# Performance work log

Measured on AMD Instinct MI355X. Metric: run time of the kernel, lower is better.

The kernel has to match this reference:

```python
import jax, jax.numpy as jnp
import numpy as np

B, F, FO, J, H, IN, OUT = 256, 16, 32, 22, 8, 256, 512
HID = OUT // H    # 64
HS = HID // 2     # 32 (spatial/temporal half)
NEG = -1e9


def setup_inputs() -> dict:
    key = jax.random.key(0)
    ks = jax.random.split(key, 10)
    s = 0.02
    f32 = jnp.float32
    return {
        "q": jax.random.normal(ks[0], (B, FO, J, IN), f32),
        "k": jax.random.normal(ks[1], (B, F, J, IN), f32),
        "v": jax.random.normal(ks[2], (B, F, J, IN), f32),
        "mask_s": jax.random.randint(ks[3], (J, J), 0, 2, jnp.int32),
        "mask_t": jax.random.randint(ks[4], (FO, FO), 0, 2, jnp.int32),
        "Wq_w": jax.random.normal(ks[5], (IN, OUT), f32) * s,
        "Wq_b": jnp.zeros((OUT,), f32),
        "Wk_w": jax.random.normal(ks[6], (IN, OUT), f32) * s,
        "Wk_b": jnp.zeros((OUT,), f32),
        "Wv_w": jax.random.normal(ks[7], (IN, OUT), f32) * s,
        "Wv_b": jnp.zeros((OUT,), f32),
        "conv_s_w": jax.random.normal(ks[8], (FO, F), f32) * s,  # 1x1 Conv2d over frame channels
        "conv_s_b": jnp.zeros((FO,), f32),
        "conv_t_w": jax.random.normal(ks[9], (FO, F), f32) * s,
        "conv_t_b": jnp.zeros((FO,), f32),
    }


def _forward(q, k, v, mask_s, mask_t, Wq_w, Wq_b, Wk_w, Wk_b, Wv_w, Wv_b,
             conv_s_w, conv_s_b, conv_t_w, conv_t_b):
    b = q.shape[0]
    temporal_size = q.shape[1]  # torch: q.shape[1] AFTER Wq -> num_frames_out
    q = q @ Wq_w + Wq_b
    k = k @ Wk_w + Wk_b
    v = v @ Wv_w + Wv_b
    # raw reshapes, exactly as the torch module (not a standard head split)
    q = q.reshape(b, H, FO, J, HID)
    k = k.reshape(b, H, F, J, HID)
    v = v.reshape(b, H, F, J, HID)
    q_s, q_t = q[..., :HS], q[..., HS:]
    k_s, k_t = k[..., :HS], k[..., HS:]
    v_s, v_t = v[..., :HS], v[..., HS:]

    def explode_s(x):
        # (b,H,F,J,HS) -> merge heads into channels -> 1x1 conv over frames -> (b,H,FO,J,HS)
        x = x.transpose(0, 2, 3, 1, 4).reshape(b, F, J, H * HS)
        x = jnp.einsum('of,bfjc->bojc', conv_s_w, x) + conv_s_b[None, :, None, None]
        return x.reshape(b, FO, J, H, HS).transpose(0, 3, 1, 2, 4)

    k_s = explode_s(k_s)
    v_s = explode_s(v_s)

    q_t = q_t.transpose(0, 1, 3, 2, 4)  # (b,H,J,FO,HS)
    v_t = v_t.transpose(0, 1, 3, 2, 4)  # (b,H,J,F,HS)
    kt = k_t.reshape(b * H, F, J, HS)   # torch double-permute is identity
    kt = jnp.einsum('of,nfjc->nojc', conv_t_w, kt) + conv_t_b[None, :, None, None]
    k_t = kt.reshape(b, H, FO, J, HS).transpose(0, 1, 3, 2, 4)  # (b,H,J,FO,HS)

    # faithful to torch.einsum: no shared contraction index -> outer product of sums
    attn_s = jnp.einsum('bhtsc,bhtdu->bhtsu', q_s, jnp.swapaxes(k_s, 3, 4))  # (b,H,FO,J,J)
    attn_s = jnp.where(mask_s == 0, NEG, attn_s)
    attn_t = jnp.einsum('bhstf,bhsug->bhstg', q_t, jnp.swapaxes(k_t, 3, 4))  # (b,H,J,FO,FO)
    attn_t = jnp.where(mask_t == 0, NEG, attn_t)
    attn_s = jax.nn.softmax(attn_s, axis=-1)
    attn_t = jax.nn.softmax(attn_t, axis=-1)

    # 'bhtss' takes the diagonal over the two joint axes (torch semantics)
    x_s = jnp.einsum('bhtss,bhtuf->bhtsf', attn_s, v_s)          # (b,H,FO,J,HS)
    x_t = jnp.einsum('bhstf,bhsug->bhstg', attn_t, v_t)          # (b,H,J,FO,HS)
    x_t = x_t.transpose(0, 1, 3, 2, 4)                            # (b,H,FO,J,HS)

    x_up = jnp.concatenate([x_s[:, :, :temporal_size], x_t], axis=-1)
    x_after_s = x_s[:, :, temporal_size:]                         # empty when q covers FO frames
    x_after = jnp.concatenate([x_after_s, jnp.zeros_like(x_after_s)], axis=-1)
    x = jnp.concatenate([x_up, x_after], axis=2)
    x = x.transpose(0, 2, 3, 1, 4).reshape(b, FO, J, H * HID)
    return x


def reference(q, k, v, mask_s, mask_t, Wq_w, Wq_b, Wk_w, Wk_b, Wv_w, Wv_b,
              conv_s_w, conv_s_b, conv_t_w, conv_t_b):
    return _forward(q, k, v, mask_s, mask_t, Wq_w, Wq_b, Wk_w, Wk_b, Wv_w, Wv_b,
                    conv_s_w, conv_s_b, conv_t_w, conv_t_b)
```

## Files before the change

kernel.cpp:

```cpp
#include <hip/hip_runtime.h>


#define NEGV (-1000000000.0f)

typedef __attribute__((ext_vector_type(8))) short short8;
typedef __attribute__((ext_vector_type(4))) float f32x4;

__device__ inline ushort f2bf(float f) {
  union { float f; unsigned u; } a;
  a.f = f;
  unsigned u = a.u;
  return (ushort)((u + 0x7FFFu + ((u >> 16) & 1u)) >> 16);
}

#define PUTG(g, pa, pb)                                                        \
  {                                                                            \
    int row_ = (g) >> 5, gl_ = (g) & 31;                                       \
    int gp_ = gl_ ^ (row_ & 7);                                                \
    short8 u_;                                                                 \
    u_[0] = (short)f2bf(pa[0]); u_[1] = (short)f2bf(pa[1]);                    \
    u_[2] = (short)f2bf(pa[2]); u_[3] = (short)f2bf(pa[3]);                    \
    u_[4] = (short)f2bf(pb[0]); u_[5] = (short)f2bf(pb[1]);                    \
    u_[6] = (short)f2bf(pb[2]); u_[7] = (short)f2bf(pb[3]);                    \
    *reinterpret_cast<short8*>(&lA[row_ * 256 + gp_ * 8]) = u_;                \
  }

#define STAGE44_NT(SRCPTR)                                                     \
  {                                                                            \
    const float* vsrc_ = (SRCPTR);                                             \
    int g0 = tid, g1 = tid + 512, g2 = tid + 1024;                             \
    f32x4 a0 = __builtin_nontemporal_load(                                     \
        reinterpret_cast<const f32x4*>(vsrc_ + g0 * 8));                       \
    f32x4 b0 = __builtin_nontemporal_load(                                     \
        reinterpret_cast<const f32x4*>(vsrc_ + g0 * 8 + 4));                   \
    f32x4 a1 = __builtin_nontemporal_load(                                     \
        reinterpret_cast<const f32x4*>(vsrc_ + g1 * 8));                       \
    f32x4 b1 = __builtin_nontemporal_load(                                     \
        reinterpret_cast<const f32x4*>(vsrc_ + g1 * 8 + 4));                   \
    f32x4 a2 = {0, 0, 0, 0}, b2 = {0, 0, 0, 0};                                \
    if (g2 < 1408) {                                                           \
      a2 = __builtin_nontemporal_load(                                         \
          reinterpret_cast<const f32x4*>(vsrc_ + g2 * 8));                     \
      b2 = __builtin_nontemporal_load(                                         \
          reinterpret_cast<const f32x4*>(vsrc_ + g2 * 8 + 4));                 \
    }                                                                          \
    PUTG(g0, a0, b0);                                                          \
    PUTG(g1, a1, b1);                                                          \
    if (g2 < 1408) PUTG(g2, a2, b2);                                           \
    if (tid < 128) {                                                           \
      int g = 1408 + tid;                                                      \
      int row_ = g >> 5, gp_ = (g & 31) ^ (row_ & 7);                          \
      short8 z = {0, 0, 0, 0, 0, 0, 0, 0};                                     \
      *reinterpret_cast<short8*>(&lA[row_ * 256 + gp_ * 8]) = z;               \
    }                                                                          \
  }

__global__ __launch_bounds__(512) void prep_all_kernel(const float* __restrict__ Wq_w,
                                                       const float* __restrict__ Wq_b,
                                                       const float* __restrict__ Wk_w,
                                                       const float* __restrict__ Wk_b,
                                                       const float* __restrict__ Wv_w,
                                                       ushort* __restrict__ qwf,
                                                       ushort* __restrict__ kwf,
                                                       ushort* __restrict__ wvtf,
                                                       float* __restrict__ sqb,
                                                       float* __restrict__ skb) {
  int bx = blockIdx.x, tid = threadIdx.x;
  if (bx < 256) {
    int idx = bx * 512 + tid;
    int e = idx & 7;
    int lane = (idx >> 3) & 63;
    int ks = (idx >> 9) & 7;
    int nt = idx >> 12;
    int r0 = lane & 15, kb = lane >> 4;
    int k = ks * 32 + kb * 8 + e;
    int ch = nt * 16 + r0;
    wvtf[idx] = f2bf(Wv_w[k * 512 + ch]);
  } else if (bx < 272) {
    int idx = (bx - 256) * 512 + tid;
    int which = idx >> 12;
    int r = idx & 4095;
    int e = r & 7;
    int lane = (r >> 3) & 63;
    int ks = r >> 9;
    int m = lane & 15, kb = lane >> 4;
    int k = ks * 32 + kb * 8 + e;
    float s = 0.f;
    if (m < 8) {
      const float* W = which ? Wk_w : Wq_w;
      const float4* p = reinterpret_cast<const float4*>(W + (size_t)k * 512 + m * 64);
      #pragma unroll
      for (int c4 = 0; c4 < 8; ++c4) {
        float4 x = p[c4];
        s += x.x + x.y + x.z + x.w;
      }
    }
    (which ? kwf : qwf)[r] = f2bf(s);
  } else {
    if (tid < 8) {
      float s = 0.f;
      for (int c = 0; c < 32; ++c) s += Wq_b[tid * 64 + c];
      sqb[tid] = s;
    } else if (tid < 16) {
      int mm = tid - 8;
      float s = 0.f;
      for (int c = 0; c < 32; ++c) s += Wk_b[mm * 64 + c];
      skb[mm] = s;
    }
  }
}

__global__ __launch_bounds__(512, 2) void fused2_kernel(const float* __restrict__ q,
                                                        const float* __restrict__ k,
                                                        const float* __restrict__ v,
                                                        const ushort* __restrict__ qwf,
                                                        const ushort* __restrict__ kwf,
                                                        const ushort* __restrict__ wvtf,
                                                        const float* __restrict__ sqb,
                                                        const float* __restrict__ skb,
                                                        const float* __restrict__ Wv_b,
                                                        float* __restrict__ qsum,
                                                        float* __restrict__ ksumraw,
                                                        float* __restrict__ vs_inner,
                                                        float* __restrict__ vtsum) {
  int bx = blockIdx.x;
  __shared__ float sbuf[6656];
  int tid = threadIdx.x, lane = tid & 63, w = tid >> 6;
  int r0 = lane & 15, kb = lane >> 4;

  bool isQK = (bx >= 4096) || !(bx & 1);
  if (isQK) {
    int gid = (bx >= 4096) ? (2048 + bx - 4096) : (bx >> 1);
    int tile = gid * 8 + w;
    bool isK = tile >= 11264;
    int tt = isK ? tile - 11264 : tile;
    const float* src = (isK ? k : q) + (size_t)(tt * 16 + r0) * 256;
    const ushort* wf = isK ? kwf : qwf;
    f32x4 acc = {0.f, 0.f, 0.f, 0.f};
    #pragma unroll
    for (int ks = 0; ks < 8; ++ks) {
      f32x4 xa = __builtin_nontemporal_load(
          reinterpret_cast<const f32x4*>(src + ks * 32 + kb * 8));
      f32x4 xb = __builtin_nontemporal_load(
          reinterpret_cast<const f32x4*>(src + ks * 32 + kb * 8 + 4));
      short8 a;
      a[0] = (short)f2bf(xa[0]); a[1] = (short)f2bf(xa[1]);
      a[2] = (short)f2bf(xa[2]); a[3] = (short)f2bf(xa[3]);
      a[4] = (short)f2bf(xb[0]); a[5] = (short)f2bf(xb[1]);
      a[6] = (short)f2bf(xb[2]); a[7] = (short)f2bf(xb[3]);
      short8 bf = *reinterpret_cast<const short8*>(wf + (ks * 64 + lane) * 8);
      acc = __builtin_amdgcn_mfma_f32_16x16x32_bf16(a, bf, acc, 0, 0, 0);
    }
    if (r0 < 8) {
      int m = r0;
      float bias = isK ? skb[m] : sqb[m];
      #pragma unroll
      for (int reg = 0; reg < 4; ++reg) {
        int R = tt * 16 + kb * 4 + reg;
        if (!isK) {
          int b = R / 704, rem = R % 704;
          int fo2 = rem / 22, j2 = rem % 22;
          int lf = (fo2 & 3) * 11264 + j2 * 512 + m * 64;
          int t = lf / 1408;
          int s = (lf % 1408) >> 6;
          int h = fo2 >> 2;
          qsum[(((size_t)b * 8 + h) * 32 + t) * 22 + s] = acc[reg] + bias;
        } else {
          int b = R / 352, rem = R % 352;
          int f2 = rem / 22, j2 = rem % 22;
          int lf = (f2 & 1) * 11264 + j2 * 512 + m * 64;
          int floc = lf / 1408;
          int jj = (lf % 1408) >> 6;
          int h = f2 >> 1;
          ksumraw[(((size_t)b * 8 + h) * 16 + floc) * 22 + jj] = acc[reg] + bias;
        }
      }
    }
  } else {
    int bh = bx >> 1;
    ushort* lA = reinterpret_cast<ushort*>(sbuf);
    float* dump = sbuf;
    STAGE44_NT(v + (size_t)bh * 11264);
    __syncthreads();

    int nt0 = w * 4;
    f32x4 acc[3][4];
    #pragma unroll
    for (int m = 0; m < 3; ++m)
      #pragma unroll
      for (int n = 0; n < 4; ++n) acc[m][n] = (f32x4){0.f, 0.f, 0.f, 0.f};

    #pragma unroll
    for (int ks = 0; ks < 8; ++ks) {
      int go = ((ks * 4 + kb) ^ (r0 & 7)) * 8;
      short8 a0 = *reinterpret_cast<const short8*>(&lA[(r0) * 256 + go]);
      short8 a1 = *reinterpret_cast<const short8*>(&lA[(16 + r0) * 256 + go]);
      short8 a2 = *reinterpret_cast<const short8*>(&lA[(32 + r0) * 256 + go]);
      #pragma unroll
      for (int n = 0; n < 4; ++n) {
        short8 bf = *reinterpret_cast<const short8*>(
            wvtf + ((size_t)((nt0 + n) * 8 + ks) * 64 + lane) * 8);
        acc[0][n] = __builtin_amdgcn_mfma_f32_16x16x32_bf16(bf, a0, acc[0][n], 0, 0, 0);
        acc[1][n] = __builtin_amdgcn_mfma_f32_16x16x32_bf16(bf, a1, acc[1][n], 0, 0, 0);
        acc[2][n] = __builtin_amdgcn_mfma_f32_16x16x32_bf16(bf, a2, acc[2][n], 0, 0, 0);
      }
    }
    __syncthreads();

    #pragma unroll
    for (int n = 0; n < 4; ++n) {
      float4 bq = *reinterpret_cast<const float4*>(Wv_b + w * 64 + n * 16 + kb * 4);
      int dbase = tid * 13;
      #pragma unroll
      for (int m = 0; m < 3; ++m) {
        dump[dbase + m * 4 + 0] = acc[m][n][0] + bq.x;
        dump[dbase + m * 4 + 1] = acc[m][n][1] + bq.y;
        dump[dbase + m * 4 + 2] = acc[m][n][2] + bq.z;
        dump[dbase + m * 4 + 3] = acc[m][n][3] + bq.w;
      }
      __syncthreads();
      if (n < 2) {
        if (tid < 256) {
          int f = tid >> 4, rest = tid & 15;
          int kb2 = rest >> 2, reg = rest & 3;
          float s = 0.f;
          #pragma unroll
          for (int u = 0; u < 22; ++u) {
            int fj = f * 22 + u;
            int f2 = (fj >= 176) ? 1 : 0;
            int rem = fj - f2 * 176;
            int j = rem >> 3, ww = rem & 7;
            int vrow = f2 * 22 + j;
            int m = vrow >> 4, rr = vrow & 15;
            s += dump[(ww * 64 + kb2 * 16 + rr) * 13 + m * 4 + reg];
          }
          vs_inner[(size_t)bh * 512 + f * 32 + n * 16 + kb2 * 4 + reg] = s;
        }
      } else {
        if (tid < 352) {
          int jj = tid >> 4, rest = tid & 15;
          int kb2 = rest >> 2, reg = rest & 3;
          float s = 0.f;
          #pragma unroll
          for (int f = 0; f < 16; ++f) {
            int fj = f * 22 + jj;
            int f2 = (fj >= 176) ? 1 : 0;
            int rem = fj - f2 * 176;
            int j = rem >> 3, ww = rem & 7;
            int vrow = f2 * 22 + j;
            int m = vrow >> 4, rr = vrow & 15;
            s += dump[(ww * 64 + kb2 * 16 + rr) * 13 + m * 4 + reg];
          }
          vtsum[(size_t)bh * 704 + jj * 32 + (n - 2) * 16 + kb2 * 4 + reg] = s;
        }
      }
      __syncthreads();
    }
  }
}

__global__ __launch_bounds__(512, 2) void final2_kernel(const float* __restrict__ qsum,
                                                        const float* __restrict__ ksumraw,
                                                        const float* __restrict__ vs_inner,
                                                        const float* __restrict__ vtsum,
                                                        const int* __restrict__ mask_s,
                                                        const float* __restrict__ csw,
                                                        const float* __restrict__ csb,
                                                        float* __restrict__ out) {
  int blk = blockIdx.x;
  int b = blk & 255, tp = blk >> 8;
  int t0 = tp * 2;
  __shared__ float vtl[8][704];
  __shared__ float vsi[8][16][32];
  __shared__ float kraw[8][16][22];
  __shared__ float ql2[2][8][22];
  __shared__ float klrow[2][8][22];
  __shared__ float vss[2][8][32];
  __shared__ float dg2[2][8][22];
  __shared__ float lcw[2][18];
  __shared__ int msk[484];
  int tid = threadIdx.x;
  size_t bb = (size_t)b;

  {
    const float4* p = reinterpret_cast<const float4*>(vtsum + bb * 5632);
    float4* dst = reinterpret_cast<float4*>(&vtl[0][0]);
    for (int i = tid; i < 1408; i += 512) dst[i] = p[i];
  }
  {
    const float4* p = reinterpret_cast<const float4*>(vs_inner + bb * 4096);
    float4* dst = reinterpret_cast<float4*>(&vsi[0][0][0]);
    for (int i = tid; i < 1024; i += 512) dst[i] = p[i];
  }
  {
    const float4* p = reinterpret_cast<const float4*>(ksumraw + bb * 2816);
    float4* dst = reinterpret_cast<float4*>(&kraw[0][0][0]);
    for (int i = tid; i < 704; i += 512) dst[i] = p[i];
  }
  if (tid < 352) {
    int tt = tid / 176, r = tid % 176;
    int h = r / 22, s = r % 22;
    ql2[tt][h][s] = qsum[((bb * 8 + h) * 32 + t0 + tt) * 22 + s];
  }
  if (tid < 484) msk[tid] = mask_s[tid];
  if (tid < 32) {
    int tt = tid >> 4, f = tid & 15;
    lcw[tt][f] = csw[(t0 + tt) * 16 + f];
  }
  if (tid >= 32 && tid < 34) lcw[tid - 32][16] = csb[t0 + (tid - 32)];
  __syncthreads();

  if (tid < 352) {
    int tt = tid / 176, r = tid % 176;
    int h = r / 22, j = r % 22;
    float a = 32.0f * lcw[tt][16];
    #pragma unroll
    for (int f = 0; f < 16; ++f) a += lcw[tt][f] * kraw[h][f][j];
    klrow[tt][h][j] = a;
  }
  {
    int tt = tid >> 8, r = tid & 255;
    int h = r >> 5, d = r & 31;
    float a = 22.0f * lcw[tt][16];
    #pragma unroll
    for (int f = 0; f < 16; ++f) a += lcw[tt][f] * vsi[h][f][d];
    vss[tt][h][d] = a;
  }
  __syncthreads();

  if (tid < 352) {
    int tt = tid / 176, r = tid % 176;
    int h = r / 22, s = r % 22;
    float qv = ql2[tt][h][s];
    float mx = -3.0e38f;
    #pragma unroll
    for (int u = 0; u < 22; ++u) {
      float av = msk[s * 22 + u] ? qv * klrow[tt][h][u] : NEGV;
      mx = fmaxf(mx, av);
    }
    float den = 0.f;
    #pragma unroll
    for (int u = 0; u < 22; ++u) {
      float av = msk[s * 22 + u] ? qv * klrow[tt][h][u] : NEGV;
      den += expf(av - mx);
    }
    float as = msk[s * 22 + s] ? qv * klrow[tt][h][s] : NEGV;
    dg2[tt][h][s] = expf(as - mx) / den;
  }
  __syncthreads();

  #pragma unroll
  for (int tt = 0; tt < 2; ++tt) {
    f32x4* ob4 = reinterpret_cast<f32x4*>(out + (size_t)(b * 32 + t0 + tt) * 11264);
    #pragma unroll
    for (int it = 0; it < 6; ++it) {
      int i4 = tid + it * 512;
      if (i4 < 2816) {
        int s = i4 >> 7;
        int ch4 = i4 & 127;
        int h = ch4 >> 4;
        int d0 = (ch4 & 15) * 4;
        f32x4 val;
        if (d0 < 32) {
          float g = dg2[tt][h][s];
          const float* vp = &vss[tt][h][d0];
          val[0] = g * vp[0]; val[1] = g * vp[1]; val[2] = g * vp[2]; val[3] = g * vp[3];
        } else {
          const float* tpn = &vtl[h][s * 32 + d0 - 32];
          val[0] = tpn[0]; val[1] = tpn[1]; val[2] = tpn[2]; val[3] = tpn[3];
        }
        __builtin_nontemporal_store(val, &ob4[i4]);
      }
    }
  }
}

extern "C" void kernel_launch(void* const* d_in, const int* in_sizes, int n_in,
                              void* d_out, int out_size, void* d_ws, size_t ws_size,
                              hipStream_t stream) {
  const float* q = (const float*)d_in[0];
  const float* k = (const float*)d_in[1];
  const float* v = (const float*)d_in[2];
  const int* mask_s = (const int*)d_in[3];
  const float* Wq_w = (const float*)d_in[5];
  const float* Wq_b = (const float*)d_in[6];
  const float* Wk_w = (const float*)d_in[7];
  const float* Wk_b = (const float*)d_in[8];
  const float* Wv_w = (const float*)d_in[9];
  const float* Wv_b = (const float*)d_in[10];
  const float* csw = (const float*)d_in[11];
  const float* csb = (const float*)d_in[12];
  float* out = (float*)d_out;

  float* ws = (float*)d_ws;
  float* sqb = ws;
  float* skb = ws + 8;
  ushort* wvtf = (ushort*)(ws + 16);
  ushort* qwf = (ushort*)(ws + 65552);
  ushort* kwf = (ushort*)(ws + 67600);
  float* qsum = ws + 69648;
  float* ksumraw = qsum + 1441792;
  float* vs_inner = ksumraw + 720896;
  float* vtsum = vs_inner + 1048576;

  hipLaunchKernelGGL(prep_all_kernel, dim3(273), dim3(512), 0, stream,
                     Wq_w, Wq_b, Wk_w, Wk_b, Wv_w, qwf, kwf, wvtf, sqb, skb);
  hipLaunchKernelGGL(fused2_kernel, dim3(4160), dim3(512), 0, stream,
                     q, k, v, qwf, kwf, wvtf, sqb, skb, Wv_b,
                     qsum, ksumraw, vs_inner, vtsum);
  hipLaunchKernelGGL(final2_kernel, dim3(4096), dim3(512), 0, stream,
                     qsum, ksumraw, vs_inner, vtsum, mask_s, csw, csb, out);
}
```

Before: 215.6 us.

## Fuse projection and final attention kernels into one per-(batch,head) mega kernel

Merges the projection/reduction kernel and the final softmax/output kernel into a single kernel with one block per (batch, head). The q/k row sums, V spatial and temporal reductions, and conv mixing now stay in shared memory instead of going through global workspace buffers. This removes one launch and the global round-trip of intermediates. In exchange the grid drops from 4160 and 4096 blocks to 2048, the Q/K projection runs on only 9 wave-tiles per block (one extra serial pass on wave 0), and shared memory use per block goes up, which may reduce occupancy.

```diff
diff --git a/kernel.cpp b/kernel.cpp
--- a/kernel.cpp
+++ b/kernel.cpp
@@ -110,31 +110,56 @@
   }
 }
 
-__global__ __launch_bounds__(512, 2) void fused2_kernel(const float* __restrict__ q,
-                                                        const float* __restrict__ k,
-                                                        const float* __restrict__ v,
-                                                        const ushort* __restrict__ qwf,
-                                                        const ushort* __restrict__ kwf,
-                                                        const ushort* __restrict__ wvtf,
-                                                        const float* __restrict__ sqb,
-                                                        const float* __restrict__ skb,
-                                                        const float* __restrict__ Wv_b,
-                                                        float* __restrict__ qsum,
-                                                        float* __restrict__ ksumraw,
-                                                        float* __restrict__ vs_inner,
-                                                        float* __restrict__ vtsum) {
-  int bx = blockIdx.x;
+__global__ __launch_bounds__(512, 2) void mega_kernel(const float* __restrict__ q,
+                                                      const float* __restrict__ k,
+                                                      const float* __restrict__ v,
+                                                      const ushort* __restrict__ qwf,
+                                                      const ushort* __restrict__ kwf,
+                                                      const ushort* __restrict__ wvtf,
+                                                      const float* __restrict__ sqb,
+                                                      const float* __restrict__ skb,
+                                                      const float* __restrict__ Wv_b,
+                                                      const float* __restrict__ csw,
+                                                      const float* __restrict__ csb,
+                                                      const int* __restrict__ mask_s,
+                                                      float* __restrict__ out) {
+  int bh = blockIdx.x;
+  int b = bh >> 3, h = bh & 7;
   __shared__ float sbuf[6656];
+  __shared__ float qs[32][23];
+  __shared__ float kraw[16][23];
+  __shared__ float kss[32][23];
+  __shared__ float vsg[16][33];
+  __shared__ float vss[32][33];
+  __shared__ float vtl[22][33];
+  __shared__ float dg[32][23];
+  __shared__ float lcsw[32][17];
+  __shared__ int msk[484];
+  ushort* lA = reinterpret_cast<ushort*>(sbuf);
+  float* dump = sbuf;
   int tid = threadIdx.x, lane = tid & 63, w = tid >> 6;
   int r0 = lane & 15, kb = lane >> 4;
 
-  bool isQK = (bx >= 4096) || !(bx & 1);
-  if (isQK) {
-    int gid = (bx >= 4096) ? (2048 + bx - 4096) : (bx >> 1);
-    int tile = gid * 8 + w;
-    bool isK = tile >= 11264;
-    int tt = isK ? tile - 11264 : tile;
-    const float* src = (isK ? k : q) + (size_t)(tt * 16 + r0) * 256;
+  STAGE44_NT(v + (size_t)bh * 11264);
+
+  if (tid < 484) msk[tid] = mask_s[tid];
+  {
+    int t = tid >> 4, f = tid & 15;
+    lcsw[t][f] = csw[t * 16 + f];
+  }
+  if (tid < 32) lcsw[tid][16] = csb[tid];
+
+  const float* qbase = q + (size_t)(b * 704 + 4 * h * 22) * 256;
+  const float* kbase = k + (size_t)(b * 352 + 2 * h * 22) * 256;
+  for (int pass = 0; pass < 2; ++pass) {
+    int u = pass == 0 ? w : 8;
+    if (pass == 1 && w != 0) break;
+    bool isK = u >= 6;
+    int ut = isK ? u - 6 : u;
+    int limit = isK ? 44 : 88;
+    int rr = ut * 16 + r0;
+    if (rr >= limit) rr = 0;
+    const float* src = (isK ? kbase : qbase) + (size_t)rr * 256;
     const ushort* wf = isK ? kwf : qwf;
     f32x4 acc = {0.f, 0.f, 0.f, 0.f};
     #pragma unroll
@@ -156,222 +181,158 @@
       float bias = isK ? skb[m] : sqb[m];
       #pragma unroll
       for (int reg = 0; reg < 4; ++reg) {
-        int R = tt * 16 + kb * 4 + reg;
-        if (!isK) {
-          int b = R / 704, rem = R % 704;
-          int fo2 = rem / 22, j2 = rem % 22;
-          int lf = (fo2 & 3) * 11264 + j2 * 512 + m * 64;
-          int t = lf / 1408;
-          int s = (lf % 1408) >> 6;
-          int h = fo2 >> 2;
-          qsum[(((size_t)b * 8 + h) * 32 + t) * 22 + s] = acc[reg] + bias;
-        } else {
-          int b = R / 352, rem = R % 352;
-          int f2 = rem / 22, j2 = rem % 22;
-          int lf = (f2 & 1) * 11264 + j2 * 512 + m * 64;
-          int floc = lf / 1408;
-          int jj = (lf % 1408) >> 6;
-          int h = f2 >> 1;
-          ksumraw[(((size_t)b * 8 + h) * 16 + floc) * 22 + jj] = acc[reg] + bias;
+        int R = ut * 16 + kb * 4 + reg;
+        if (R < limit) {
+          if (!isK) {
+            int fo2l = R / 22, j2 = R % 22;
+            int lf = fo2l * 11264 + j2 * 512 + m * 64;
+            int t = lf / 1408;
+            int s = (lf % 1408) >> 6;
+            qs[t][s] = acc[reg] + bias;
+          } else {
+            int f2l = R / 22, j2 = R % 22;
+            int lf = f2l * 11264 + j2 * 512 + m * 64;
+            int floc = lf / 1408;
+            int jj = (lf % 1408) >> 6;
+            kraw[floc][jj] = acc[reg] + bias;
+          }
         }
       }
     }
-  } else {
-    int bh = bx >> 1;
-    ushort* lA = reinterpret_cast<ushort*>(sbuf);
-    float* dump = sbuf;
-    STAGE44_NT(v + (size_t)bh * 11264);
+  }
+  __syncthreads();
+
+  int nt0 = w * 4;
+  f32x4 acc[3][4];
+  #pragma unroll
+  for (int m = 0; m < 3; ++m)
+    #pragma unroll
+    for (int n = 0; n < 4; ++n) acc[m][n] = (f32x4){0.f, 0.f, 0.f, 0.f};
+
+  #pragma unroll
+  for (int ks = 0; ks < 8; ++ks) {
+    int go = ((ks * 4 + kb) ^ (r0 & 7)) * 8;
+    short8 a0 = *reinterpret_cast<const short8*>(&lA[(r0) * 256 + go]);
+    short8 a1 = *reinterpret_cast<const short8*>(&lA[(16 + r0) * 256 + go]);
+    short8 a2 = *reinterpret_cast<const short8*>(&lA[(32 + r0) * 256 + go]);
+    #pragma unroll
+    for (int n = 0; n < 4; ++n) {
+      short8 bf = *reinterpret_cast<const short8*>(
+          wvtf + ((size_t)((nt0 + n) * 8 + ks) * 64 + lane) * 8);
+      acc[0][n] = __builtin_amdgcn_mfma_f32_16x16x32_bf16(bf, a0, acc[0][n], 0, 0, 0);
+      acc[1][n] = __builtin_amdgcn_mfma_f32_16x16x32_bf16(bf, a1, acc[1][n], 0, 0, 0);
+      acc[2][n] = __builtin_amdgcn_mfma_f32_16x16x32_bf16(bf, a2, acc[2][n], 0, 0, 0);
+    }
+  }
+  __syncthreads();
+
+  #pragma unroll
+  for (int n = 0; n < 4; ++n) {
+    float4 bq = *reinterpret_cast<const float4*>(Wv_b + w * 64 + n * 16 + kb * 4);
+    int dbase = tid * 13;
+    #pragma unroll
+    for (int m = 0; m < 3; ++m) {
+      dump[dbase + m * 4 + 0] = acc[m][n][0] + bq.x;
+      dump[dbase + m * 4 + 1] = acc[m][n][1] + bq.y;
+      dump[dbase + m * 4 + 2] = acc[m][n][2] + bq.z;
+      dump[dbase + m * 4 + 3] = acc[m][n][3] + bq.w;
+    }
     __syncthreads();
-
-    int nt0 = w * 4;
-    f32x4 acc[3][4];
-    #pragma unroll
-    for (int m = 0; m < 3; ++m)
-      #pragma unroll
-      for (int n = 0; n < 4; ++n) acc[m][n] = (f32x4){0.f, 0.f, 0.f, 0.f};
-
-    #pragma unroll
-    for (int ks = 0; ks < 8; ++ks) {
-      int go = ((ks * 4 + kb) ^ (r0 & 7)) * 8;
-      short8 a0 = *reinterpret_cast<const short8*>(&lA[(r0) * 256 + go]);
-      short8 a1 = *reinterpret_cast<const short8*>(&lA[(16 + r0) * 256 + go]);
-      short8 a2 = *reinterpret_cast<const short8*>(&lA[(32 + r0) * 256 + go]);
-      #pragma unroll
-      for (int n = 0; n < 4; ++n) {
-        short8 bf = *reinterpret_cast<const short8*>(
-            wvtf + ((size_t)((nt0 + n) * 8 + ks) * 64 + lane) * 8);
-        acc[0][n] = __builtin_amdgcn_mfma_f32_16x16x32_bf16(bf, a0, acc[0][n], 0, 0, 0);
-        acc[1][n] = __builtin_amdgcn_mfma_f32_16x16x32_bf16(bf, a1, acc[1][n], 0, 0, 0);
-        acc[2][n] = __builtin_amdgcn_mfma_f32_16x16x32_bf16(bf, a2, acc[2][n], 0, 0, 0);
+    if (n < 2) {
+      if (tid < 256) {
+        int f = tid >> 4, rest = tid & 15;
+        int kb2 = rest >> 2, reg = rest & 3;
+        float s = 0.f;
+        #pragma unroll
+        for (int u = 0; u < 22; ++u) {
+          int fj = f * 22 + u;
+          int f2 = (fj >= 176) ? 1 : 0;
+          int rem = fj - f2 * 176;
+          int j = rem >> 3, ww = rem & 7;
+          int vrow = f2 * 22 + j;
+          int m = vrow >> 4, rr2 = vrow & 15;
+          s += dump[(ww * 64 + kb2 * 16 + rr2) * 13 + m * 4 + reg];
+        }
+        vsg[f][n * 16 + kb2 * 4 + reg] = s;
       }
+    } else {
+      if (tid < 352) {
+        int jj = tid >> 4, rest = tid & 15;
+        int kb2 = rest >> 2, reg = rest & 3;
+        float s = 0.f;
+        #pragma unroll
+        for (int f = 0; f < 16; ++f) {
+          int fj = f * 22 + jj;
+          int f2 = (fj >= 176) ? 1 : 0;
+          int rem = fj - f2 * 176;
+          int j = rem >> 3, ww = rem & 7;
+          int vrow = f2 * 22 + j;
+          int m = vrow >> 4, rr2 = vrow & 15;
+          s += dump[(ww * 64 + kb2 * 16 + rr2) * 13 + m * 4 + reg];
+        }
+        vtl[jj][(n - 2) * 16 + kb2 * 4 + reg] = s;
+      }
     }
     __syncthreads();
-
-    #pragma unroll
-    for (int n = 0; n < 4; ++n) {
-      float4 bq = *reinterpret_cast<const float4*>(Wv_b + w * 64 + n * 16 + kb * 4);
-      int dbase = tid * 13;
-      #pragma unroll
-      for (int m = 0; m < 3; ++m) {
-        dump[dbase + m * 4 + 0] = acc[m][n][0] + bq.x;
-        dump[dbase + m * 4 + 1] = acc[m][n][1] + bq.y;
-        dump[dbase + m * 4 + 2] = acc[m][n][2] + bq.z;
-        dump[dbase + m * 4 + 3] = acc[m][n][3] + bq.w;
-      }
-      __syncthreads();
-      if (n < 2) {
-        if (tid < 256) {
-          int f = tid >> 4, rest = tid & 15;
-          int kb2 = rest >> 2, reg = rest & 3;
-          float s = 0.f;
-          #pragma unroll
-          for (int u = 0; u < 22; ++u) {
-            int fj = f * 22 + u;
-            int f2 = (fj >= 176) ? 1 : 0;
-            int rem = fj - f2 * 176;
-            int j = rem >> 3, ww = rem & 7;
-            int vrow = f2 * 22 + j;
-            int m = vrow >> 4, rr = vrow & 15;
-            s += dump[(ww * 64 + kb2 * 16 + rr) * 13 + m * 4 + reg];
-          }
-          vs_inner[(size_t)bh * 512 + f * 32 + n * 16 + kb2 * 4 + reg] = s;
-        }
-      } else {
-        if (tid < 352) {
-          int jj = tid >> 4, rest = tid & 15;
-          int kb2 = rest >> 2, reg = rest & 3;
-          float s = 0.f;
-          #pragma unroll
-          for (int f = 0; f < 16; ++f) {
-            int fj = f * 22 + jj;
-            int f2 = (fj >= 176) ? 1 : 0;
-            int rem = fj - f2 * 176;
-            int j = rem >> 3, ww = rem & 7;
-            int vrow = f2 * 22 + j;
-            int m = vrow >> 4, rr = vrow & 15;
-            s += dump[(ww * 64 + kb2 * 16 + rr) * 13 + m * 4 + reg];
-          }
-          vtsum[(size_t)bh * 704 + jj * 32 + (n - 2) * 16 + kb2 * 4 + reg] = s;
-        }
-      }
-      __syncthreads();
-    }
-  }
-}
-
-__global__ __launch_bounds__(512, 2) void final2_kernel(const float* __restrict__ qsum,
-                                                        const float* __restrict__ ksumraw,
-                                                        const float* __restrict__ vs_inner,
-                                                        const float* __restrict__ vtsum,
-                                                        const int* __restrict__ mask_s,
-                                                        const float* __restrict__ csw,
-                                                        const float* __restrict__ csb,
-                                                        float* __restrict__ out) {
-  int blk = blockIdx.x;
-  int b = blk & 255, tp = blk >> 8;
-  int t0 = tp * 2;
-  __shared__ float vtl[8][704];
-  __shared__ float vsi[8][16][32];
-  __shared__ float kraw[8][16][22];
-  __shared__ float ql2[2][8][22];
-  __shared__ float klrow[2][8][22];
-  __shared__ float vss[2][8][32];
-  __shared__ float dg2[2][8][22];
-  __shared__ float lcw[2][18];
-  __shared__ int msk[484];
-  int tid = threadIdx.x;
-  size_t bb = (size_t)b;
-
+  }
+
+  for (int o = tid; o < 704; o += 512) {
+    int t = o / 22, j = o % 22;
+    float a = 32.0f * lcsw[t][16];
+    #pragma unroll
+    for (int f = 0; f < 16; ++f) a += lcsw[t][f] * kraw[f][j];
+    kss[t][j] = a;
+  }
   {
-    const float4* p = reinterpret_cast<const float4*>(vtsum + bb * 5632);
-    float4* dst = reinterpret_cast<float4*>(&vtl[0][0]);
-    for (int i = tid; i < 1408; i += 512) dst[i] = p[i];
-  }
-  {
-    const float4* p = reinterpret_cast<const float4*>(vs_inner + bb * 4096);
-    float4* dst = reinterpret_cast<float4*>(&vsi[0][0][0]);
-    for (int i = tid; i < 1024; i += 512) dst[i] = p[i];
-  }
-  {
-    const float4* p = reinterpret_cast<const float4*>(ksumraw + bb * 2816);
-    float4* dst = reinterpret_cast<float4*>(&kraw[0][0][0]);
-    for (int i = tid; i < 704; i += 512) dst[i] = p[i];
-  }
-  if (tid < 352) {
-    int tt = tid / 176, r = tid % 176;
-    int h = r / 22, s = r % 22;
-    ql2[tt][h][s] = qsum[((bb * 8 + h) * 32 + t0 + tt) * 22 + s];
-  }
-  if (tid < 484) msk[tid] = mask_s[tid];
-  if (tid < 32) {
-    int tt = tid >> 4, f = tid & 15;
-    lcw[tt][f] = csw[(t0 + tt) * 16 + f];
-  }
-  if (tid >= 32 && tid < 34) lcw[tid - 32][16] = csb[t0 + (tid - 32)];
+    int t = tid >> 4, d2 = (tid & 15) * 2;
+    float a0 = 22.0f * lcsw[t][16], a1 = a0;
+    #pragma unroll
+    for (int f = 0; f < 16; ++f) {
+      float cw = lcsw[t][f];
+      a0 += cw * vsg[f][d2];
+      a1 += cw * vsg[f][d2 + 1];
+    }
+    vss[t][d2] = a0;
+    vss[t][d2 + 1] = a1;
+  }
   __syncthreads();
 
-  if (tid < 352) {
-    int tt = tid / 176, r = tid % 176;
-    int h = r / 22, j = r % 22;
-    float a = 32.0f * lcw[tt][16];
-    #pragma unroll
-    for (int f = 0; f < 16; ++f) a += lcw[tt][f] * kraw[h][f][j];
-    klrow[tt][h][j] = a;
-  }
-  {
-    int tt = tid >> 8, r = tid & 255;
-    int h = r >> 5, d = r & 31;
-    float a = 22.0f * lcw[tt][16];
-    #pragma unroll
-    for (int f = 0; f < 16; ++f) a += lcw[tt][f] * vsi[h][f][d];
-    vss[tt][h][d] = a;
+  for (int p = tid; p < 704; p += 512) {
+    int t = p / 22, s = p % 22;
+    float qv = qs[t][s];
+    float mx = -3.0e38f;
+    #pragma unroll
+    for (int u = 0; u < 22; ++u) {
+      float av = msk[s * 22 + u] ? qv * kss[t][u] : NEGV;
+      mx = fmaxf(mx, av);
+    }
+    float den = 0.f;
+    #pragma unroll
+    for (int u = 0; u < 22; ++u) {
+      float av = msk[s * 22 + u] ? qv * kss[t][u] : NEGV;
+      den += expf(av - mx);
+    }
+    float as = msk[s * 22 + s] ? qv * kss[t][s] : NEGV;
+    dg[t][s] = expf(as - mx) / den;
   }
   __syncthreads();
 
-  if (tid < 352) {
-    int tt = tid / 176, r = tid % 176;
-    int h = r / 22, s = r % 22;
-    float qv = ql2[tt][h][s];
-    float mx = -3.0e38f;
-    #pragma unroll
-    for (int u = 0; u < 22; ++u) {
-      float av = msk[s * 22 + u] ? qv * klrow[tt][h][u] : NEGV;
-      mx = fmaxf(mx, av);
-    }
-    float den = 0.f;
-    #pragma unroll
-    for (int u = 0; u < 22; ++u) {
-      float av = msk[s * 22 + u] ? qv * klrow[tt][h][u] : NEGV;
-      den += expf(av - mx);
-    }
-    float as = msk[s * 22 + s] ? qv * klrow[tt][h][s] : NEGV;
-    dg2[tt][h][s] = expf(as - mx) / den;
-  }
-  __syncthreads();
-
-  #pragma unroll
-  for (int tt = 0; tt < 2; ++tt) {
-    f32x4* ob4 = reinterpret_cast<f32x4*>(out + (size_t)(b * 32 + t0 + tt) * 11264);
-    #pragma unroll
-    for (int it = 0; it < 6; ++it) {
-      int i4 = tid + it * 512;
-      if (i4 < 2816) {
-        int s = i4 >> 7;
-        int ch4 = i4 & 127;
-        int h = ch4 >> 4;
-        int d0 = (ch4 & 15) * 4;
-        f32x4 val;
-        if (d0 < 32) {
-          float g = dg2[tt][h][s];
-          const float* vp = &vss[tt][h][d0];
-          val[0] = g * vp[0]; val[1] = g * vp[1]; val[2] = g * vp[2]; val[3] = g * vp[3];
-        } else {
-          const float* tpn = &vtl[h][s * 32 + d0 - 32];
-          val[0] = tpn[0]; val[1] = tpn[1]; val[2] = tpn[2]; val[3] = tpn[3];
-        }
-        __builtin_nontemporal_store(val, &ob4[i4]);
-      }
-    }
+  float* ob = out + (size_t)b * 32 * 22 * 512 + h * 64;
+  for (int i = tid; i < 11264; i += 512) {
+    int ts = i >> 4, w4 = i & 15;
+    int t = ts / 22, s = ts % 22;
+    int d0 = w4 * 4;
+    f32x4 val;
+    if (d0 < 32) {
+      float g = dg[t][s];
+      const float* vp = &vss[t][d0];
+      val[0] = g * vp[0]; val[1] = g * vp[1]; val[2] = g * vp[2]; val[3] = g * vp[3];
+    } else {
+      const float* tp = &vtl[s][d0 - 32];
+      val[0] = tp[0]; val[1] = tp[1]; val[2] = tp[2]; val[3] = tp[3];
+    }
+    __builtin_nontemporal_store(
+        val, reinterpret_cast<f32x4*>(ob + (size_t)(t * 22 + s) * 512 + d0));
   }
 }
 
@@ -398,16 +359,9 @@
   ushort* wvtf = (ushort*)(ws + 16);
   ushort* qwf = (ushort*)(ws + 65552);
   ushort* kwf = (ushort*)(ws + 67600);
-  float* qsum = ws + 69648;
-  float* ksumraw = qsum + 1441792;
-  float* vs_inner = ksumraw + 720896;
-  float* vtsum = vs_inner + 1048576;
 
   hipLaunchKernelGGL(prep_all_kernel, dim3(273), dim3(512), 0, stream,
                      Wq_w, Wq_b, Wk_w, Wk_b, Wv_w, qwf, kwf, wvtf, sqb, skb);
-  hipLaunchKernelGGL(fused2_kernel, dim3(4160), dim3(512), 0, stream,
-                     q, k, v, qwf, kwf, wvtf, sqb, skb, Wv_b,
-                     qsum, ksumraw, vs_inner, vtsum);
-  hipLaunchKernelGGL(final2_kernel, dim3(4096), dim3(512), 0, stream,
-                     qsum, ksumraw, vs_inner, vtsum, mask_s, csw, csb, out);
+  hipLaunchKernelGGL(mega_kernel, dim3(2048), dim3(512), 0, stream,
+                     q, k, v, qwf, kwf, wvtf, sqb, skb, Wv_b, csw, csb, mask_s, out);
 }
```

New measurement: 205.7 us. -4.6%, faster.
